# Kernel tuning notes

Hardware: AMD Instinct MI355X
Metric: run time of the kernel (lower is better)

Reference implementation:

```python
import jax, jax.numpy as jnp
import numpy as np

B, N, C_IN, C_OUT = 8, 4096, 64, 64
NEG_INF = -9e15
LEAKY_SLOPE = 0.01  # torch F.leaky_relu default


def setup_inputs() -> dict:
    key = jax.random.key(0)
    kx, ka, kw, kq, kk = jax.random.split(key, 5)
    X = jax.random.normal(kx, (B, N, C_IN), dtype=jnp.float32)
    A = jax.random.randint(ka, (N, N), 0, 2, dtype=jnp.int32)
    # xavier_uniform with gain=1.414 ~ scaled uniform; plain scaled normal is fine for a numeric reference
    def xavier(k, shape):
        fan_in, fan_out = shape
        bound = 1.414 * np.sqrt(6.0 / (fan_in + fan_out))
        return jax.random.uniform(k, shape, jnp.float32, -bound, bound)
    weight = xavier(kw, (C_IN, C_OUT))
    query = xavier(kq, (C_IN, C_OUT))
    key_p = xavier(kk, (C_IN, C_OUT))
    return {"X": X, "A": A, "weight": weight, "query": query, "key_p": key_p}


def reference(X, A, weight, query, key_p):
    n = X.shape[1]
    idx = jnp.arange(n)
    adj = A.at[idx, idx].set(1)  # add self-loops
    out = jnp.einsum('bni,io->bno', X, weight)
    q = jnp.einsum('bni,io->bno', X, query)
    k = jnp.einsum('bni,io->bno', X, key_p)
    att = jnp.einsum('bnd,bmd->bnm', q, k)          # QK^T, (B,N,N)
    att = jax.nn.leaky_relu(att, LEAKY_SLOPE)
    att = jnp.where(adj[None, :, :] > 0, att, NEG_INF)
    att = jax.nn.softmax(att, axis=-1)
    # dropout p=0 and/or eval mode -> identity
    return jnp.einsum('bnm,bmo->bno', att, out)
```

## Files before the change

kernel.cpp:

```cpp
#include <hip/hip_runtime.h>
#include <stdint.h>

#define BATCH 8
#define NN 4096
#define CC 64
#define MASKV -1.0e30f
#define LOG2E 1.4426950408889634f

typedef _Float16 half8 __attribute__((ext_vector_type(8)));
typedef __fp16 fp16x2 __attribute__((ext_vector_type(2)));
typedef float f32x4 __attribute__((ext_vector_type(4)));

__global__ __launch_bounds__(256) void gat_proj(
    const float* __restrict__ X, const float* __restrict__ W0,
    const float* __restrict__ Wq, const float* __restrict__ Wk,
    _Float16* __restrict__ qh,
    _Float16* __restrict__ kb, _Float16* __restrict__ vt)
{
    __shared__ alignas(16) _Float16 WTh[3][64][72];
    __shared__ alignas(16) _Float16 WTl[3][64][72];
    const int t = threadIdx.x;
    const float* Ws[3] = {W0, Wq, Wk};
    for (int e = t; e < 4096; e += 256) {
        int k = e >> 6, c = e & 63;
        #pragma unroll
        for (int m = 0; m < 3; ++m) {
            float w = Ws[m][e];
            _Float16 hi = (_Float16)w;
            WTh[m][c][k] = hi;
            WTl[m][c][k] = (_Float16)(w - (float)hi);
        }
    }
    __syncthreads();
    const int lane = t & 63, wv = t >> 6;
    const int cl = lane & 15, g = lane >> 4;
    {
        int tile = blockIdx.x * 4 + wv;
        int gr = tile * 16;
        const float* xr = X + (size_t)(gr + cl) * CC;
        half8 xh[2], xl[2];
        #pragma unroll
        for (int kf = 0; kf < 2; ++kf) {
            f32x4 a0 = *(const f32x4*)(xr + g*8 + kf*32);
            f32x4 a1 = *(const f32x4*)(xr + g*8 + kf*32 + 4);
            half8 h, l;
            #pragma unroll
            for (int j = 0; j < 4; ++j) {
                _Float16 h0 = (_Float16)a0[j], h1 = (_Float16)a1[j];
                h[j]   = h0; l[j]   = (_Float16)(a0[j] - (float)h0);
                h[j+4] = h1; l[j+4] = (_Float16)(a1[j] - (float)h1);
            }
            xh[kf] = h; xl[kf] = l;
        }
        #pragma unroll
        for (int mat = 1; mat <= 2; ++mat) {
            #pragma unroll
            for (int nt = 0; nt < 4; ++nt) {
                f32x4 acc = {0.f, 0.f, 0.f, 0.f};
                #pragma unroll
                for (int kf = 0; kf < 2; ++kf) {
                    half8 bh = *(const half8*)&WTh[mat][nt*16 + cl][g*8 + kf*32];
                    half8 bl = *(const half8*)&WTl[mat][nt*16 + cl][g*8 + kf*32];
                    acc = __builtin_amdgcn_mfma_f32_16x16x32_f16(xh[kf], bh, acc, 0, 0, 0);
                    acc = __builtin_amdgcn_mfma_f32_16x16x32_f16(xl[kf], bh, acc, 0, 0, 0);
                    acc = __builtin_amdgcn_mfma_f32_16x16x32_f16(xh[kf], bl, acc, 0, 0, 0);
                }
                #pragma unroll
                for (int i = 0; i < 4; ++i) {
                    size_t off = (size_t)(gr + 4*g + i) * CC + nt*16 + cl;
                    if (mat == 1) {
                        qh[off] = (_Float16)(acc[i] * LOG2E);
                    } else {
                        kb[off] = (_Float16)acc[i];
                    }
                }
            }
        }
        {
            int b = gr >> 12, n0 = gr & (NN - 1);
            #pragma unroll
            for (int mt = 0; mt < 4; ++mt) {
                f32x4 acc = {0.f, 0.f, 0.f, 0.f};
                #pragma unroll
                for (int kf = 0; kf < 2; ++kf) {
                    half8 ah = *(const half8*)&WTh[0][mt*16 + cl][g*8 + kf*32];
                    half8 al = *(const half8*)&WTl[0][mt*16 + cl][g*8 + kf*32];
                    acc = __builtin_amdgcn_mfma_f32_16x16x32_f16(ah, xh[kf], acc, 0, 0, 0);
                    acc = __builtin_amdgcn_mfma_f32_16x16x32_f16(al, xh[kf], acc, 0, 0, 0);
                    acc = __builtin_amdgcn_mfma_f32_16x16x32_f16(ah, xl[kf], acc, 0, 0, 0);
                }
                #pragma unroll
                for (int i = 0; i < 4; ++i) {
                    int co = mt*16 + 4*g + i;
                    vt[((size_t)b * CC + co) * NN + n0 + cl] = (_Float16)acc[i];
                }
            }
        }
    }
}

__global__ __launch_bounds__(256) void gat_mask(const int* __restrict__ A,
                                                unsigned short* __restrict__ M16)
{
    const int row = blockIdx.x;
    const int w16 = threadIdx.x;
    const int4* ap = (const int4*)(A + (size_t)row * NN + w16 * 16);
    unsigned m = 0;
    #pragma unroll
    for (int j = 0; j < 4; ++j) {
        int4 a = ap[j];
        m |= (a.x != 0 ? 1u : 0u) << (4*j);
        m |= (a.y != 0 ? 1u : 0u) << (4*j + 1);
        m |= (a.z != 0 ? 1u : 0u) << (4*j + 2);
        m |= (a.w != 0 ? 1u : 0u) << (4*j + 3);
    }
    if (w16 == (row >> 4)) m |= 1u << (row & 15);
    M16[(size_t)row * 256 + w16] = (unsigned short)m;
}

__global__ __launch_bounds__(256) void gat_attn(
    const _Float16* __restrict__ qg,
    const _Float16* __restrict__ kf16, const _Float16* __restrict__ vtb,
    const unsigned long long* __restrict__ M,
    _Float16* __restrict__ po, float2* __restrict__ pml)
{
    __shared__ alignas(16) _Float16 Kt[64][64];
    __shared__ alignas(16) _Float16 Vt[64][64];
    __shared__ alignas(16) _Float16 Ps[4][32][64];
    __shared__ alignas(8) uint2 LUT[16];
    const int t = threadIdx.x;
    const int lane = t & 63, wv = t >> 6;
    const int cl = lane & 15, g = lane >> 4;
    const int blk = blockIdx.x;
    const int b  = blk & 7;
    const int sp = (blk >> 3) & 3;
    const int qb = blk >> 5;
    const int Q0 = qb * 128 + wv * 32;
    const int c0 = sp * 16;
    const int swz = (cl & 7) << 4;

    if (t < 16) {
        unsigned n = t;
        LUT[n] = make_uint2(((n & 1u) ? 0x0000FFFFu : 0u) | ((n & 2u) ? 0xFFFF0000u : 0u),
                            ((n & 4u) ? 0x0000FFFFu : 0u) | ((n & 8u) ? 0xFFFF0000u : 0u));
    }

    const int soff = (((t >> 3) * 128 + (t & 7) * 16) ^ (((t >> 3) & 7) << 4));
    char* const kd0 = (char*)Kt + soff;
    char* const kd1 = (char*)Kt + soff + 32 * 128;
    char* const vd0 = (char*)Vt + soff;
    char* const vd1 = (char*)Vt + soff + 32 * 128;
    char* const psb = (char*)&Ps[wv][0][0];

    half8 qf[2][2];
    #pragma unroll
    for (int qt = 0; qt < 2; ++qt) {
        const _Float16* qr = qg + ((size_t)b * NN + Q0 + qt*16 + cl) * CC;
        qf[qt][0] = *(const half8*)(qr + g*8);
        qf[qt][1] = *(const half8*)(qr + g*8 + 32);
    }
    const _Float16* kg = kf16 + (size_t)b * NN * CC;
    const _Float16* vg = vtb + (size_t)b * CC * NN;

    f32x4 o[2][4] = {};
    float m_run[2] = {MASKV, MASKV}, l_run[2] = {0.f, 0.f};

    uint4 pk0, pk1, pv0, pv1;
    unsigned long long pmA, pmB;
    auto loadchunk = [&](int kc) {
        const uint4* ks = (const uint4*)(kg + (size_t)kc * 64 * CC);
        pk0 = ks[t];
        pk1 = ks[t + 256];
        const _Float16* vs = vg + kc * 64;
        pv0 = *(const uint4*)(vs + (size_t)(t >> 3) * NN + (t & 7) * 8);
        pv1 = *(const uint4*)(vs + (size_t)((t >> 3) + 32) * NN + (t & 7) * 8);
        pmA = M[(size_t)(Q0 + cl) * 64 + kc];
        pmB = M[(size_t)(Q0 + 16 + cl) * 64 + kc];
    };
    loadchunk(c0);

    auto pkmax = [](unsigned a, unsigned b) {
        unsigned d;
        asm("v_pk_max_f16 %0, %1, %2" : "=v"(d) : "v"(a), "v"(b));
        return d;
    };

    for (int kc = 0; kc < 16; ++kc) {
        __syncthreads();
        *(uint4*)kd0 = pk0;
        *(uint4*)kd1 = pk1;
        *(uint4*)vd0 = pv0;
        *(uint4*)vd1 = pv1;
        const unsigned long long cmA = pmA, cmB = pmB;
        __syncthreads();
        if (kc < 15) loadchunk(c0 + kc + 1);

        __builtin_amdgcn_s_setprio(1);
        f32x4 sc[2][4] = {};
        #pragma unroll
        for (int kt = 0; kt < 4; ++kt) {
            #pragma unroll
            for (int kf = 0; kf < 2; ++kf) {
                half8 ka = *(const half8*)((char*)Kt +
                    ((((kt*16 + cl) * 128) + g*16 + kf*64) ^ swz));
                sc[0][kt] = __builtin_amdgcn_mfma_f32_16x16x32_f16(ka, qf[0][kf], sc[0][kt], 0, 0, 0);
                sc[1][kt] = __builtin_amdgcn_mfma_f32_16x16x32_f16(ka, qf[1][kf], sc[1][kt], 0, 0, 0);
            }
        }
        __builtin_amdgcn_s_setprio(0);

        #pragma unroll
        for (int qt = 0; qt < 2; ++qt) {
            const unsigned long long cm = qt ? cmB : cmA;
            const unsigned wlo = (unsigned)cm, whi = (unsigned)(cm >> 32);
            unsigned hm[8];
            #pragma unroll
            for (int kt = 0; kt < 4; ++kt) {
                unsigned w = (kt < 2) ? wlo : whi;
                unsigned nib = (w >> ((kt & 1) * 16 + 4 * g)) & 15u;
                uint2 e = LUT[nib];
                hm[2*kt]   = e.x;
                hm[2*kt+1] = e.y;
            }
            float sv[16];
            #pragma unroll
            for (int j = 0; j < 16; ++j) {
                float x = sc[qt][j >> 2][j & 3];
                sv[j] = fmaxf(x, 0.01f * x);
            }
            union UH { unsigned u; fp16x2 h; };
            unsigned sm[8];
            #pragma unroll
            for (int kt = 0; kt < 4; ++kt) {
                UH s0, s1;
                s0.h = __builtin_amdgcn_cvt_pkrtz(sv[4*kt + 0], sv[4*kt + 1]);
                s1.h = __builtin_amdgcn_cvt_pkrtz(sv[4*kt + 2], sv[4*kt + 3]);
                sm[2*kt]   = (hm[2*kt]   & s0.u) | (~hm[2*kt]   & 0xFC00FC00u);
                sm[2*kt+1] = (hm[2*kt+1] & s1.u) | (~hm[2*kt+1] & 0xFC00FC00u);
            }
            unsigned tm = pkmax(
                pkmax(pkmax(sm[0], sm[1]), pkmax(sm[2], sm[3])),
                pkmax(pkmax(sm[4], sm[5]), pkmax(sm[6], sm[7])));
            UH tmu; tmu.u = tm;
            float mx = fmaxf((float)tmu.h[0], (float)tmu.h[1]);
            mx = fmaxf(mx, __shfl_xor(mx, 16));
            mx = fmaxf(mx, __shfl_xor(mx, 32));
            if (__any(mx > m_run[qt])) {
                float nm = fmaxf(m_run[qt], mx);
                float alpha = __builtin_amdgcn_exp2f(m_run[qt] - nm);
                m_run[qt] = nm;
                l_run[qt] *= alpha;
                #pragma unroll
                for (int ct = 0; ct < 4; ++ct) o[qt][ct] *= alpha;
            }
            float p[16];
            #pragma unroll
            for (int j = 0; j < 16; ++j)
                p[j] = __builtin_amdgcn_exp2f(sv[j] - m_run[qt]);
            UH zz; zz.u = 0u;
            fp16x2 acc2 = zz.h;
            #pragma unroll
            for (int kt = 0; kt < 4; ++kt) {
                UH w0, w1;
                w0.h = __builtin_amdgcn_cvt_pkrtz(p[kt*4 + 0], p[kt*4 + 1]);
                w1.h = __builtin_amdgcn_cvt_pkrtz(p[kt*4 + 2], p[kt*4 + 3]);
                w0.u &= hm[2*kt];
                w1.u &= hm[2*kt+1];
                uint2 pw = {w0.u, w1.u};
                *(uint2*)(psb + ((((qt*16 + cl) * 128) + kt*32 + g*8) ^ swz)) = pw;
                acc2 += w0.h + w1.h;
            }
            l_run[qt] += (float)acc2[0] + (float)acc2[1];

            __builtin_amdgcn_wave_barrier();

            half8 pf0 = *(const half8*)(psb + ((((qt*16 + cl) * 128) + g*16) ^ swz));
            half8 pf1 = *(const half8*)(psb + ((((qt*16 + cl) * 128) + g*16 + 64) ^ swz));
            __builtin_amdgcn_s_setprio(1);
            #pragma unroll
            for (int ct = 0; ct < 4; ++ct) {
                half8 vf0 = *(const half8*)((char*)Vt + ((((ct*16 + cl) * 128) + g*16) ^ swz));
                half8 vf1 = *(const half8*)((char*)Vt + ((((ct*16 + cl) * 128) + g*16 + 64) ^ swz));
                o[qt][ct] = __builtin_amdgcn_mfma_f32_16x16x32_f16(vf0, pf0, o[qt][ct], 0, 0, 0);
                o[qt][ct] = __builtin_amdgcn_mfma_f32_16x16x32_f16(vf1, pf1, o[qt][ct], 0, 0, 0);
            }
            __builtin_amdgcn_s_setprio(0);
        }
    }

    #pragma unroll
    for (int qt = 0; qt < 2; ++qt) {
        float lt = l_run[qt];
        lt += __shfl_xor(lt, 16);
        lt += __shfl_xor(lt, 32);
        size_t base = (size_t)sp * (BATCH * NN) + (size_t)b * NN + Q0 + qt*16 + cl;
        _Float16* orow = po + base * 64;
        #pragma unroll
        for (int ct = 0; ct < 4; ++ct) {
            union { fp16x2 h; unsigned u; } o0u, o1u;
            o0u.h = __builtin_amdgcn_cvt_pkrtz(o[qt][ct][0], o[qt][ct][1]);
            o1u.h = __builtin_amdgcn_cvt_pkrtz(o[qt][ct][2], o[qt][ct][3]);
            uint2 ow = {o0u.u, o1u.u};
            *(uint2*)(orow + ct*16 + 4*g) = ow;
        }
        if (g == 0) pml[base] = make_float2(m_run[qt], lt);
    }
}

__global__ __launch_bounds__(256) void gat_comb(
    const _Float16* __restrict__ po, const float2* __restrict__ pml,
    float* __restrict__ out)
{
    int gid = blockIdx.x * 256 + threadIdx.x;
    int row = gid >> 2;
    int col = (gid & 3) * 16;
    float2 ml[4];
    float Mx = MASKV;
    #pragma unroll
    for (int s = 0; s < 4; ++s) {
        ml[s] = pml[s * (BATCH * NN) + row];
        Mx = fmaxf(Mx, ml[s].x);
    }
    float w[4], den = 0.f;
    #pragma unroll
    for (int s = 0; s < 4; ++s) {
        w[s] = __builtin_amdgcn_exp2f(ml[s].x - Mx);
        den += w[s] * ml[s].y;
    }
    float inv = 1.0f / den;
    float acc[16] = {};
    #pragma unroll
    for (int s = 0; s < 4; ++s) {
        const _Float16* p = po + ((size_t)s * (BATCH * NN) + row) * 64 + col;
        float a = w[s] * inv;
        half8 v0 = *(const half8*)(p);
        half8 v1 = *(const half8*)(p + 8);
        #pragma unroll
        for (int j = 0; j < 8; ++j) {
            acc[j]     += a * (float)v0[j];
            acc[j + 8] += a * (float)v1[j];
        }
    }
    float* op = out + (size_t)row * 64 + col;
    #pragma unroll
    for (int i = 0; i < 4; ++i) {
        f32x4 r = {acc[4*i], acc[4*i+1], acc[4*i+2], acc[4*i+3]};
        *(f32x4*)(op + i*4) = r;
    }
}

extern "C" void kernel_launch(void* const* d_in, const int* in_sizes, int n_in,
                              void* d_out, int out_size, void* d_ws, size_t ws_size,
                              hipStream_t stream) {
    const float* X  = (const float*)d_in[0];
    const int*   A  = (const int*)d_in[1];
    const float* W0 = (const float*)d_in[2];
    const float* Wq = (const float*)d_in[3];
    const float* Wk = (const float*)d_in[4];
    float* out = (float*)d_out;
    char* ws = (char*)d_ws;
    const size_t SZ = (size_t)BATCH * NN * CC * 2;
    _Float16* qh  = (_Float16*)(ws);
    _Float16* kbf = (_Float16*)(ws + SZ);
    _Float16* vtb = (_Float16*)(ws + 2*SZ);
    char* Mbase = ws + 3*SZ;
    _Float16* po = (_Float16*)(Mbase + 2*1024*1024);
    float2* pml  = (float2*)(Mbase + 2*1024*1024 + 4*SZ);

    hipLaunchKernelGGL(gat_proj, dim3(512),  dim3(256), 0, stream, X, W0, Wq, Wk, qh, kbf, vtb);
    hipLaunchKernelGGL(gat_mask, dim3(4096), dim3(256), 0, stream, A, (unsigned short*)Mbase);
    hipLaunchKernelGGL(gat_attn, dim3(1024), dim3(256), 0, stream, qh, kbf, vtb,
                       (const unsigned long long*)Mbase, po, pml);
    hipLaunchKernelGGL(gat_comb, dim3(512),  dim3(256), 0, stream, po, pml, out);
}
```

Measured before the change: 203.6 us.

## Switch attention kernel to 32x32x16 MFMA with double-buffered LDS and register P

```diff
diff --git a/kernel.cpp b/kernel.cpp
--- a/kernel.cpp
+++ b/kernel.cpp
@@ -10,6 +10,13 @@
 typedef _Float16 half8 __attribute__((ext_vector_type(8)));
 typedef __fp16 fp16x2 __attribute__((ext_vector_type(2)));
 typedef float f32x4 __attribute__((ext_vector_type(4)));
+typedef float f32x16 __attribute__((ext_vector_type(16)));
+
+__device__ __forceinline__ unsigned pk_rtz(float a, float b) {
+    union { fp16x2 h; unsigned u; } r;
+    r.h = __builtin_amdgcn_cvt_pkrtz(a, b);
+    return r.u;
+}
 
 __global__ __launch_bounds__(256) void gat_proj(
     const float* __restrict__ X, const float* __restrict__ W0,
@@ -68,11 +75,8 @@
                 #pragma unroll
                 for (int i = 0; i < 4; ++i) {
                     size_t off = (size_t)(gr + 4*g + i) * CC + nt*16 + cl;
-                    if (mat == 1) {
-                        qh[off] = (_Float16)(acc[i] * LOG2E);
-                    } else {
-                        kb[off] = (_Float16)acc[i];
-                    }
+                    if (mat == 1) qh[off] = (_Float16)(acc[i] * LOG2E);
+                    else          kb[off] = (_Float16)acc[i];
                 }
             }
         }
@@ -124,20 +128,19 @@
     const unsigned long long* __restrict__ M,
     _Float16* __restrict__ po, float2* __restrict__ pml)
 {
-    __shared__ alignas(16) _Float16 Kt[64][64];
-    __shared__ alignas(16) _Float16 Vt[64][64];
-    __shared__ alignas(16) _Float16 Ps[4][32][64];
+    __shared__ alignas(16) _Float16 Kt[2][64][64];
+    __shared__ alignas(16) _Float16 Vt[2][64][64];
     __shared__ alignas(8) uint2 LUT[16];
     const int t = threadIdx.x;
     const int lane = t & 63, wv = t >> 6;
-    const int cl = lane & 15, g = lane >> 4;
+    const int q32 = lane & 31, hi = lane >> 5;
     const int blk = blockIdx.x;
     const int b  = blk & 7;
     const int sp = (blk >> 3) & 3;
     const int qb = blk >> 5;
     const int Q0 = qb * 128 + wv * 32;
     const int c0 = sp * 16;
-    const int swz = (cl & 7) << 4;
+    const int swz = (q32 & 7) << 4;
 
     if (t < 16) {
         unsigned n = t;
@@ -146,165 +149,170 @@
     }
 
     const int soff = (((t >> 3) * 128 + (t & 7) * 16) ^ (((t >> 3) & 7) << 4));
-    char* const kd0 = (char*)Kt + soff;
-    char* const kd1 = (char*)Kt + soff + 32 * 128;
-    char* const vd0 = (char*)Vt + soff;
-    char* const vd1 = (char*)Vt + soff + 32 * 128;
-    char* const psb = (char*)&Ps[wv][0][0];
-
-    half8 qf[2][2];
-    #pragma unroll
-    for (int qt = 0; qt < 2; ++qt) {
-        const _Float16* qr = qg + ((size_t)b * NN + Q0 + qt*16 + cl) * CC;
-        qf[qt][0] = *(const half8*)(qr + g*8);
-        qf[qt][1] = *(const half8*)(qr + g*8 + 32);
+
+    half8 qf[4];
+    {
+        const _Float16* qr = qg + ((size_t)b * NN + Q0 + q32) * CC + hi * 8;
+        #pragma unroll
+        for (int kf = 0; kf < 4; ++kf) qf[kf] = *(const half8*)(qr + kf * 16);
     }
     const _Float16* kg = kf16 + (size_t)b * NN * CC;
     const _Float16* vg = vtb + (size_t)b * CC * NN;
 
-    f32x4 o[2][4] = {};
-    float m_run[2] = {MASKV, MASKV}, l_run[2] = {0.f, 0.f};
+    f32x16 o0 = {}, o1 = {};
+    float m_run = 0.f, l_run = 0.f;
 
     uint4 pk0, pk1, pv0, pv1;
-    unsigned long long pmA, pmB;
-    auto loadchunk = [&](int kc) {
-        const uint4* ks = (const uint4*)(kg + (size_t)kc * 64 * CC);
+    unsigned long long pm;
+    auto loadchunk = [&](int kcg) {
+        const uint4* ks = (const uint4*)(kg + (size_t)kcg * 64 * CC);
         pk0 = ks[t];
         pk1 = ks[t + 256];
-        const _Float16* vs = vg + kc * 64;
+        const _Float16* vs = vg + kcg * 64;
         pv0 = *(const uint4*)(vs + (size_t)(t >> 3) * NN + (t & 7) * 8);
         pv1 = *(const uint4*)(vs + (size_t)((t >> 3) + 32) * NN + (t & 7) * 8);
-        pmA = M[(size_t)(Q0 + cl) * 64 + kc];
-        pmB = M[(size_t)(Q0 + 16 + cl) * 64 + kc];
+        pm  = M[(size_t)(Q0 + q32) * 64 + kcg];
     };
-    loadchunk(c0);
-
+    auto stash = [&](int bufi) {
+        char* kd = (char*)&Kt[bufi][0][0];
+        char* vd = (char*)&Vt[bufi][0][0];
+        *(uint4*)(kd + soff) = pk0;
+        *(uint4*)(kd + soff + 4096) = pk1;
+        *(uint4*)(vd + soff) = pv0;
+        *(uint4*)(vd + soff + 4096) = pv1;
+    };
     auto pkmax = [](unsigned a, unsigned b) {
         unsigned d;
         asm("v_pk_max_f16 %0, %1, %2" : "=v"(d) : "v"(a), "v"(b));
         return d;
     };
 
+    loadchunk(c0);
+    unsigned long long cm = pm;
+    stash(0);
+    __syncthreads();
+
     for (int kc = 0; kc < 16; ++kc) {
-        __syncthreads();
-        *(uint4*)kd0 = pk0;
-        *(uint4*)kd1 = pk1;
-        *(uint4*)vd0 = pv0;
-        *(uint4*)vd1 = pv1;
-        const unsigned long long cmA = pmA, cmB = pmB;
-        __syncthreads();
+        const int cur = kc & 1;
         if (kc < 15) loadchunk(c0 + kc + 1);
 
+        const char* kbase = (const char*)&Kt[cur][0][0] + q32 * 128;
         __builtin_amdgcn_s_setprio(1);
-        f32x4 sc[2][4] = {};
-        #pragma unroll
-        for (int kt = 0; kt < 4; ++kt) {
-            #pragma unroll
-            for (int kf = 0; kf < 2; ++kf) {
-                half8 ka = *(const half8*)((char*)Kt +
-                    ((((kt*16 + cl) * 128) + g*16 + kf*64) ^ swz));
-                sc[0][kt] = __builtin_amdgcn_mfma_f32_16x16x32_f16(ka, qf[0][kf], sc[0][kt], 0, 0, 0);
-                sc[1][kt] = __builtin_amdgcn_mfma_f32_16x16x32_f16(ka, qf[1][kf], sc[1][kt], 0, 0, 0);
-            }
+        f32x16 s0 = {}, s1 = {};
+        #pragma unroll
+        for (int kf = 0; kf < 4; ++kf) {
+            const int col = (kf * 32 + hi * 16) ^ swz;
+            half8 ka0 = *(const half8*)(kbase + col);
+            half8 ka1 = *(const half8*)(kbase + 4096 + col);
+            s0 = __builtin_amdgcn_mfma_f32_32x32x16_f16(ka0, qf[kf], s0, 0, 0, 0);
+            s1 = __builtin_amdgcn_mfma_f32_32x32x16_f16(ka1, qf[kf], s1, 0, 0, 0);
         }
         __builtin_amdgcn_s_setprio(0);
 
-        #pragma unroll
-        for (int qt = 0; qt < 2; ++qt) {
-            const unsigned long long cm = qt ? cmB : cmA;
-            const unsigned wlo = (unsigned)cm, whi = (unsigned)(cm >> 32);
-            unsigned hm[8];
-            #pragma unroll
-            for (int kt = 0; kt < 4; ++kt) {
-                unsigned w = (kt < 2) ? wlo : whi;
-                unsigned nib = (w >> ((kt & 1) * 16 + 4 * g)) & 15u;
+        const unsigned wlo = (unsigned)cm, whi = (unsigned)(cm >> 32);
+        unsigned hm[16];
+        #pragma unroll
+        for (int kt = 0; kt < 2; ++kt) {
+            unsigned w = kt ? whi : wlo;
+            #pragma unroll
+            for (int a = 0; a < 4; ++a) {
+                unsigned nib = (w >> (8 * a + 4 * hi)) & 15u;
                 uint2 e = LUT[nib];
-                hm[2*kt]   = e.x;
-                hm[2*kt+1] = e.y;
-            }
-            float sv[16];
-            #pragma unroll
-            for (int j = 0; j < 16; ++j) {
-                float x = sc[qt][j >> 2][j & 3];
-                sv[j] = fmaxf(x, 0.01f * x);
-            }
-            union UH { unsigned u; fp16x2 h; };
-            unsigned sm[8];
-            #pragma unroll
-            for (int kt = 0; kt < 4; ++kt) {
-                UH s0, s1;
-                s0.h = __builtin_amdgcn_cvt_pkrtz(sv[4*kt + 0], sv[4*kt + 1]);
-                s1.h = __builtin_amdgcn_cvt_pkrtz(sv[4*kt + 2], sv[4*kt + 3]);
-                sm[2*kt]   = (hm[2*kt]   & s0.u) | (~hm[2*kt]   & 0xFC00FC00u);
-                sm[2*kt+1] = (hm[2*kt+1] & s1.u) | (~hm[2*kt+1] & 0xFC00FC00u);
-            }
-            unsigned tm = pkmax(
-                pkmax(pkmax(sm[0], sm[1]), pkmax(sm[2], sm[3])),
-                pkmax(pkmax(sm[4], sm[5]), pkmax(sm[6], sm[7])));
-            UH tmu; tmu.u = tm;
-            float mx = fmaxf((float)tmu.h[0], (float)tmu.h[1]);
-            mx = fmaxf(mx, __shfl_xor(mx, 16));
+                hm[kt*8 + 2*a]     = e.x;
+                hm[kt*8 + 2*a + 1] = e.y;
+            }
+        }
+        {
+            unsigned sm[16];
+            #pragma unroll
+            for (int j = 0; j < 8; ++j) {
+                sm[j]   = pk_rtz(s0[2*j], s0[2*j+1]) & hm[j];
+                sm[8+j] = pk_rtz(s1[2*j], s1[2*j+1]) & hm[8+j];
+            }
+            unsigned u0 = pkmax(pkmax(pkmax(sm[0],sm[1]),  pkmax(sm[2],sm[3])),
+                                pkmax(pkmax(sm[4],sm[5]),  pkmax(sm[6],sm[7])));
+            unsigned u1 = pkmax(pkmax(pkmax(sm[8],sm[9]),  pkmax(sm[10],sm[11])),
+                                pkmax(pkmax(sm[12],sm[13]),pkmax(sm[14],sm[15])));
+            union { unsigned u; fp16x2 h; } tu; tu.u = pkmax(u0, u1);
+            float mx = fmaxf(fmaxf((float)tu.h[0], (float)tu.h[1]), 0.f);
             mx = fmaxf(mx, __shfl_xor(mx, 32));
-            if (__any(mx > m_run[qt])) {
-                float nm = fmaxf(m_run[qt], mx);
-                float alpha = __builtin_amdgcn_exp2f(m_run[qt] - nm);
-                m_run[qt] = nm;
-                l_run[qt] *= alpha;
-                #pragma unroll
-                for (int ct = 0; ct < 4; ++ct) o[qt][ct] *= alpha;
-            }
-            float p[16];
-            #pragma unroll
-            for (int j = 0; j < 16; ++j)
-                p[j] = __builtin_amdgcn_exp2f(sv[j] - m_run[qt]);
-            UH zz; zz.u = 0u;
-            fp16x2 acc2 = zz.h;
-            #pragma unroll
-            for (int kt = 0; kt < 4; ++kt) {
-                UH w0, w1;
-                w0.h = __builtin_amdgcn_cvt_pkrtz(p[kt*4 + 0], p[kt*4 + 1]);
-                w1.h = __builtin_amdgcn_cvt_pkrtz(p[kt*4 + 2], p[kt*4 + 3]);
-                w0.u &= hm[2*kt];
-                w1.u &= hm[2*kt+1];
-                uint2 pw = {w0.u, w1.u};
-                *(uint2*)(psb + ((((qt*16 + cl) * 128) + kt*32 + g*8) ^ swz)) = pw;
-                acc2 += w0.h + w1.h;
-            }
-            l_run[qt] += (float)acc2[0] + (float)acc2[1];
-
-            __builtin_amdgcn_wave_barrier();
-
-            half8 pf0 = *(const half8*)(psb + ((((qt*16 + cl) * 128) + g*16) ^ swz));
-            half8 pf1 = *(const half8*)(psb + ((((qt*16 + cl) * 128) + g*16 + 64) ^ swz));
-            __builtin_amdgcn_s_setprio(1);
-            #pragma unroll
-            for (int ct = 0; ct < 4; ++ct) {
-                half8 vf0 = *(const half8*)((char*)Vt + ((((ct*16 + cl) * 128) + g*16) ^ swz));
-                half8 vf1 = *(const half8*)((char*)Vt + ((((ct*16 + cl) * 128) + g*16 + 64) ^ swz));
-                o[qt][ct] = __builtin_amdgcn_mfma_f32_16x16x32_f16(vf0, pf0, o[qt][ct], 0, 0, 0);
-                o[qt][ct] = __builtin_amdgcn_mfma_f32_16x16x32_f16(vf1, pf1, o[qt][ct], 0, 0, 0);
-            }
-            __builtin_amdgcn_s_setprio(0);
-        }
-    }
-
-    #pragma unroll
-    for (int qt = 0; qt < 2; ++qt) {
-        float lt = l_run[qt];
-        lt += __shfl_xor(lt, 16);
-        lt += __shfl_xor(lt, 32);
-        size_t base = (size_t)sp * (BATCH * NN) + (size_t)b * NN + Q0 + qt*16 + cl;
-        _Float16* orow = po + base * 64;
-        #pragma unroll
-        for (int ct = 0; ct < 4; ++ct) {
-            union { fp16x2 h; unsigned u; } o0u, o1u;
-            o0u.h = __builtin_amdgcn_cvt_pkrtz(o[qt][ct][0], o[qt][ct][1]);
-            o1u.h = __builtin_amdgcn_cvt_pkrtz(o[qt][ct][2], o[qt][ct][3]);
-            uint2 ow = {o0u.u, o1u.u};
-            *(uint2*)(orow + ct*16 + 4*g) = ow;
-        }
-        if (g == 0) pml[base] = make_float2(m_run[qt], lt);
-    }
+            if (__any(mx > m_run)) {
+                float nm = fmaxf(m_run, mx);
+                float alpha = __builtin_amdgcn_exp2f(m_run - nm);
+                m_run = nm;
+                l_run *= alpha;
+                #pragma unroll
+                for (int i = 0; i < 16; ++i) { o0[i] *= alpha; o1[i] *= alpha; }
+            }
+        }
+        unsigned wp[16];
+        #pragma unroll
+        for (int j = 0; j < 8; ++j) {
+            float p0 = __builtin_amdgcn_exp2f(fmaxf(s0[2*j]   - m_run, fmaf(0.01f, s0[2*j],   -m_run)));
+            float p1 = __builtin_amdgcn_exp2f(fmaxf(s0[2*j+1] - m_run, fmaf(0.01f, s0[2*j+1], -m_run)));
+            float p2 = __builtin_amdgcn_exp2f(fmaxf(s1[2*j]   - m_run, fmaf(0.01f, s1[2*j],   -m_run)));
+            float p3 = __builtin_amdgcn_exp2f(fmaxf(s1[2*j+1] - m_run, fmaf(0.01f, s1[2*j+1], -m_run)));
+            wp[j]   = pk_rtz(p0, p1) & hm[j];
+            wp[8+j] = pk_rtz(p2, p3) & hm[8+j];
+        }
+        {
+            union { unsigned u; fp16x2 h; } z; z.u = 0u;
+            fp16x2 acc = z.h;
+            #pragma unroll
+            for (int j4 = 0; j4 < 4; ++j4) {
+                union { unsigned u; fp16x2 h; } x0, x1, x2, x3;
+                x0.u = wp[4*j4]; x1.u = wp[4*j4+1]; x2.u = wp[4*j4+2]; x3.u = wp[4*j4+3];
+                acc += (x0.h + x1.h) + (x2.h + x3.h);
+            }
+            l_run += (float)acc[0] + (float)acc[1];
+        }
+        if (kc < 15) stash(cur ^ 1);
+        #pragma unroll
+        for (int g4 = 0; g4 < 4; ++g4) {
+            unsigned w0 = wp[4*g4+0], w1 = wp[4*g4+1];
+            unsigned w2 = wp[4*g4+2], w3 = wp[4*g4+3];
+            unsigned u = hi ? w0 : w2;
+            unsigned v = hi ? w1 : w3;
+            unsigned su = (unsigned)__shfl_xor((int)u, 32);
+            unsigned sv = (unsigned)__shfl_xor((int)v, 32);
+            wp[4*g4+0] = hi ? su : w0;
+            wp[4*g4+1] = hi ? sv : w1;
+            wp[4*g4+2] = hi ? w2 : su;
+            wp[4*g4+3] = hi ? w3 : sv;
+        }
+        const char* vb = (const char*)&Vt[cur][0][0] + q32 * 128;
+        __builtin_amdgcn_s_setprio(1);
+        #pragma unroll
+        for (int kc4 = 0; kc4 < 4; ++kc4) {
+            union { unsigned u[4]; half8 h; } pb;
+            pb.u[0] = wp[4*kc4+0]; pb.u[1] = wp[4*kc4+1];
+            pb.u[2] = wp[4*kc4+2]; pb.u[3] = wp[4*kc4+3];
+            const int col = (kc4 * 32 + hi * 16) ^ swz;
+            half8 vf0 = *(const half8*)(vb + col);
+            half8 vf1 = *(const half8*)(vb + 4096 + col);
+            o0 = __builtin_amdgcn_mfma_f32_32x32x16_f16(vf0, pb.h, o0, 0, 0, 0);
+            o1 = __builtin_amdgcn_mfma_f32_32x32x16_f16(vf1, pb.h, o1, 0, 0, 0);
+        }
+        __builtin_amdgcn_s_setprio(0);
+        cm = pm;
+        if (kc < 15) __syncthreads();
+    }
+
+    float lt = l_run + __shfl_xor(l_run, 32);
+    size_t base = (size_t)sp * (BATCH * NN) + (size_t)b * NN + Q0 + q32;
+    _Float16* orow = po + base * 64;
+    #pragma unroll
+    for (int a = 0; a < 4; ++a) {
+        {
+            uint2 ow = { pk_rtz(o0[4*a], o0[4*a+1]), pk_rtz(o0[4*a+2], o0[4*a+3]) };
+            *(uint2*)(orow + 8*a + 4*hi) = ow;
+        }
+        {
+            uint2 ow = { pk_rtz(o1[4*a], o1[4*a+1]), pk_rtz(o1[4*a+2], o1[4*a+3]) };
+            *(uint2*)(orow + 32 + 8*a + 4*hi) = ow;
+        }
+    }
+    if (hi == 0) pml[base] = make_float2(m_run, lt);
 }
 
 __global__ __launch_bounds__(256) void gat_comb(
```

Result: faster. 199.2 us (-2.2%).
